# Kernel optimization log

Hardware: AMD Instinct MI355X
Metric: run time of the kernel (lower is better)

Reference implementation:

```python
import jax, jax.numpy as jnp
import numpy as np

CUTOFF = 1.0  # nm
KE = 138.96   # Coulomb constant conversion factor used by the module


def physnet_attenuation(r, cutoff=CUTOFF):
    # PhysNet smooth switching function: 1 - 6u^5 + 15u^4 - 10u^3 for u<1, else 0
    u = r / cutoff
    phi = 1.0 - 6.0 * u**5 + 15.0 * u**4 - 10.0 * u**3
    return jnp.where(u < 1.0, phi, 0.0)


def setup_inputs() -> dict:
    key = jax.random.key(0)
    k1, k2, k3, k4 = jax.random.split(key, 4)
    N = 262144          # total atoms
    P = 16777216        # total pairs (~64 neighbors/atom)
    S = 1024            # number of systems
    pair_idx = jax.random.randint(k1, (2, P), 0, N, dtype=jnp.int32)
    # distances in (0.05, 1.25) nm; 2*d straddles the cutoff so both branches of chi_r are exercised
    d_ij = (jax.random.uniform(k2, (P, 1), dtype=jnp.float32) * 1.2 + 0.05)
    charge = jax.random.normal(k3, (N, 1), dtype=jnp.float32) * 0.3
    sys_idx = jnp.sort(jax.random.randint(k4, (N,), 0, S, dtype=jnp.int32))
    return {
        "electrostatic_pair_indices": pair_idx,
        "electrostatic_d_ij": d_ij,
        "per_atom_charge": charge,
        "atomic_subsystem_indices": sys_idx,
        "num_systems": S,
    }


def reference(electrostatic_pair_indices, electrostatic_d_ij, per_atom_charge,
              atomic_subsystem_indices, num_systems):
    idx_i = electrostatic_pair_indices[0]
    idx_j = electrostatic_pair_indices[1]
    # unique-pair mask (static shapes: zero out instead of filtering)
    mask = idx_i < idx_j
    d = electrostatic_d_ij[:, 0]                       # [P]
    q = per_atom_charge[:, 0]                          # [N]
    phi_2r = physnet_attenuation(2.0 * d)
    chi_r = phi_2r / jnp.sqrt(d * d + 1.0) + (1.0 - phi_2r) / d
    e_pair = q[idx_i] * q[idx_j] * chi_r               # [P]
    e_pair = jnp.where(mask, e_pair, 0.0)
    seg = atomic_subsystem_indices[idx_i]              # system of each pair
    per_system = jax.ops.segment_sum(e_pair, seg, num_segments=num_systems)
    return (per_system * KE)[:, None]                  # [S, 1]
```

## Files before the change

kernel.cpp:

```cpp
#include <hip/hip_runtime.h>

typedef int   v4i __attribute__((ext_vector_type(4)));
typedef float v4f __attribute__((ext_vector_type(4)));

#define S_SYS   1024
#define KE_CONST 138.96f
#define BLOCKS  1024
#define THREADS 256

__global__ __launch_bounds__(256) void pack_kernel(const float* __restrict__ q,
                                                   const int* __restrict__ sys,
                                                   float2* __restrict__ packed, int N) {
    int i = blockIdx.x * blockDim.x + threadIdx.x;
    if (i < N) {
        float2 v;
        v.x = q[i];
        v.y = __int_as_float(sys[i]);
        packed[i] = v;
    }
}

__global__ __launch_bounds__(256) void pair_kernel(const v4i* __restrict__ idx_i4,
                                                   const v4i* __restrict__ idx_j4,
                                                   const v4f* __restrict__ d4,
                                                   const float2* __restrict__ packed,
                                                   float* __restrict__ partial,
                                                   int P4) {
    __shared__ float acc[4][S_SYS];
    const int tid = threadIdx.x;
    const int wave = tid >> 6;
    for (int t = tid; t < 4 * S_SYS; t += THREADS) ((float*)acc)[t] = 0.0f;
    __syncthreads();

    const int stride = gridDim.x * blockDim.x;
    for (int p = blockIdx.x * blockDim.x + tid; p < P4; p += stride) {
        v4i vi = __builtin_nontemporal_load(&idx_i4[p]);
        v4i vj = __builtin_nontemporal_load(&idx_j4[p]);
        v4f vd = __builtin_nontemporal_load(&d4[p]);
#pragma unroll
        for (int k = 0; k < 4; ++k) {
            int i = vi[k], j = vj[k];
            if (i < j) {
                float d  = vd[k];
                float2 pi = packed[i];
                float qj  = packed[j].x;
                float u = 2.0f * d;
                float phi = 0.0f;
                if (u < 1.0f) {
                    float u3 = u * u * u;
                    phi = 1.0f - u3 * (10.0f + u * (6.0f * u - 15.0f));
                }
                float chi = phi * __builtin_amdgcn_rsqf(d * d + 1.0f)
                          + (1.0f - phi) * __builtin_amdgcn_rcpf(d);
                float e = pi.x * qj * chi;
                atomicAdd(&acc[wave][__float_as_int(pi.y)], e);
            }
        }
    }
    __syncthreads();
    for (int s = tid; s < S_SYS; s += THREADS) {
        float v = acc[0][s] + acc[1][s] + acc[2][s] + acc[3][s];
        partial[(size_t)blockIdx.x * S_SYS + s] = v;
    }
}

__global__ __launch_bounds__(256) void reduce_kernel(const float* __restrict__ partial,
                                                     float* __restrict__ out, int B) {
    int s = blockIdx.x;
    float sum = 0.0f;
    for (int b = threadIdx.x; b < B; b += blockDim.x)
        sum += partial[(size_t)b * S_SYS + s];
#pragma unroll
    for (int off = 32; off > 0; off >>= 1) sum += __shfl_down(sum, off, 64);
    __shared__ float wsum[4];
    if ((threadIdx.x & 63) == 0) wsum[threadIdx.x >> 6] = sum;
    __syncthreads();
    if (threadIdx.x == 0) out[s] = KE_CONST * (wsum[0] + wsum[1] + wsum[2] + wsum[3]);
}

extern "C" void kernel_launch(void* const* d_in, const int* in_sizes, int n_in,
                              void* d_out, int out_size, void* d_ws, size_t ws_size,
                              hipStream_t stream) {
    const int*   pair = (const int*)d_in[0];
    const float* d_ij = (const float*)d_in[1];
    const float* q    = (const float*)d_in[2];
    const int*   sys  = (const int*)d_in[3];
    const int P = in_sizes[1];
    const int N = in_sizes[2];
    float* out = (float*)d_out;

    float2* packed  = (float2*)d_ws;
    float*  partial = (float*)((char*)d_ws + (size_t)N * sizeof(float2));

    pack_kernel<<<(N + 255) / 256, 256, 0, stream>>>(q, sys, packed, N);

    pair_kernel<<<BLOCKS, THREADS, 0, stream>>>(
        (const v4i*)pair, (const v4i*)(pair + P), (const v4f*)d_ij,
        packed, partial, P / 4);

    reduce_kernel<<<S_SYS, 256, 0, stream>>>(partial, out, BLOCKS);
}
```

Measured before the change: 301.3 us.

## Batch two vector loads per thread and hoist gathers for memory-level parallelism

Each thread now processes two strided groups of four pairs per iteration, issuing all streaming loads and then all eight random gathers of packed charge/system data before doing the arithmetic and LDS atomics. The block size doubles to 512 threads with eight per-wave LDS histograms, and chi is rewritten as rcp + phi*(rsq - rcp) to save a multiply. The goal is more outstanding memory requests per wave to hide gather latency, at the cost of higher register pressure and twice the LDS per block, which may lower occupancy.

```diff
diff --git a/kernel.cpp b/kernel.cpp
--- a/kernel.cpp
+++ b/kernel.cpp
@@ -3,10 +3,11 @@
 typedef int   v4i __attribute__((ext_vector_type(4)));
 typedef float v4f __attribute__((ext_vector_type(4)));
 
-#define S_SYS   1024
+#define S_SYS    1024
 #define KE_CONST 138.96f
-#define BLOCKS  1024
-#define THREADS 256
+#define BLOCKS   1024
+#define THREADS  512
+#define NWAVE    (THREADS / 64)
 
 __global__ __launch_bounds__(256) void pack_kernel(const float* __restrict__ q,
                                                    const int* __restrict__ sys,
@@ -20,46 +21,74 @@
     }
 }
 
-__global__ __launch_bounds__(256) void pair_kernel(const v4i* __restrict__ idx_i4,
-                                                   const v4i* __restrict__ idx_j4,
-                                                   const v4f* __restrict__ d4,
-                                                   const float2* __restrict__ packed,
-                                                   float* __restrict__ partial,
-                                                   int P4) {
-    __shared__ float acc[4][S_SYS];
+__global__ __launch_bounds__(THREADS, 8) void pair_kernel(const v4i* __restrict__ idx_i4,
+                                                          const v4i* __restrict__ idx_j4,
+                                                          const v4f* __restrict__ d4,
+                                                          const float2* __restrict__ packed,
+                                                          float* __restrict__ partial,
+                                                          int P4) {
+    __shared__ float acc[NWAVE][S_SYS];
     const int tid = threadIdx.x;
     const int wave = tid >> 6;
-    for (int t = tid; t < 4 * S_SYS; t += THREADS) ((float*)acc)[t] = 0.0f;
+    for (int t = tid; t < NWAVE * S_SYS; t += THREADS) ((float*)acc)[t] = 0.0f;
     __syncthreads();
 
     const int stride = gridDim.x * blockDim.x;
-    for (int p = blockIdx.x * blockDim.x + tid; p < P4; p += stride) {
-        v4i vi = __builtin_nontemporal_load(&idx_i4[p]);
-        v4i vj = __builtin_nontemporal_load(&idx_j4[p]);
-        v4f vd = __builtin_nontemporal_load(&d4[p]);
+    for (int p = blockIdx.x * blockDim.x + tid; p < P4; p += 2 * stride) {
+        const int p2 = p + stride;
+        const bool has2 = (p2 < P4);
+
+        v4i vi0 = __builtin_nontemporal_load(&idx_i4[p]);
+        v4i vj0 = __builtin_nontemporal_load(&idx_j4[p]);
+        v4f vd0 = __builtin_nontemporal_load(&d4[p]);
+        v4i vi1 = {0, 0, 0, 0};
+        v4i vj1 = {0, 0, 0, 0};
+        v4f vd1 = {1.f, 1.f, 1.f, 1.f};
+        if (has2) {
+            vi1 = __builtin_nontemporal_load(&idx_i4[p2]);
+            vj1 = __builtin_nontemporal_load(&idx_j4[p2]);
+            vd1 = __builtin_nontemporal_load(&d4[p2]);
+        }
+
+        int   ii[8], jj[8];
+        float dd[8];
 #pragma unroll
-        for (int k = 0; k < 4; ++k) {
-            int i = vi[k], j = vj[k];
-            if (i < j) {
-                float d  = vd[k];
-                float2 pi = packed[i];
-                float qj  = packed[j].x;
-                float u = 2.0f * d;
+        for (int k = 0; k < 4; ++k) { ii[k] = vi0[k];     jj[k] = vj0[k];     dd[k] = vd0[k]; }
+#pragma unroll
+        for (int k = 0; k < 4; ++k) { ii[4 + k] = vi1[k]; jj[4 + k] = vj1[k]; dd[4 + k] = vd1[k]; }
+
+        float2 pi[8];
+        float  qj[8];
+#pragma unroll
+        for (int k = 0; k < 8; ++k) {
+            if (ii[k] < jj[k]) {
+                pi[k] = packed[ii[k]];
+                qj[k] = packed[jj[k]].x;
+            }
+        }
+
+#pragma unroll
+        for (int k = 0; k < 8; ++k) {
+            if (ii[k] < jj[k]) {
+                float d   = dd[k];
+                float u   = 2.0f * d;
                 float phi = 0.0f;
                 if (u < 1.0f) {
                     float u3 = u * u * u;
                     phi = 1.0f - u3 * (10.0f + u * (6.0f * u - 15.0f));
                 }
-                float chi = phi * __builtin_amdgcn_rsqf(d * d + 1.0f)
-                          + (1.0f - phi) * __builtin_amdgcn_rcpf(d);
-                float e = pi.x * qj * chi;
-                atomicAdd(&acc[wave][__float_as_int(pi.y)], e);
+                float rcp = __builtin_amdgcn_rcpf(d);
+                float chi = rcp + phi * (__builtin_amdgcn_rsqf(d * d + 1.0f) - rcp);
+                float e   = pi[k].x * qj[k] * chi;
+                atomicAdd(&acc[wave][__float_as_int(pi[k].y)], e);
             }
         }
     }
     __syncthreads();
     for (int s = tid; s < S_SYS; s += THREADS) {
-        float v = acc[0][s] + acc[1][s] + acc[2][s] + acc[3][s];
+        float v = 0.0f;
+#pragma unroll
+        for (int w = 0; w < NWAVE; ++w) v += acc[w][s];
         partial[(size_t)blockIdx.x * S_SYS + s] = v;
     }
 }
```

Measured after the change: 300.0 us. About the same (-0.4%).
